# Performance work log

Measured on AMD Instinct MI355X. Metric: run time of the kernel, lower is better.

## Reference

```python
import jax, jax.numpy as jnp
import numpy as np

KERNEL_MUL = 2.0
KERNEL_NUM = 5


def setup_inputs() -> dict:
    key = jax.random.key(0)
    k1, k2 = jax.random.split(key)
    source = jax.random.normal(k1, (4096, 256), dtype=jnp.float32)
    target = jax.random.normal(k2, (4096, 256), dtype=jnp.float32)
    return {"source": source, "target": target}


def reference(source, target):
    n = source.shape[0]
    total = jnp.concatenate([source, target], axis=0)  # [2N, D]
    ns = total.shape[0]
    # Squared-L2 pairwise distances via the GEMM trick (avoids [2N,2N,D] blowup)
    sq = jnp.sum(total * total, axis=1)  # [2N]
    dist = sq[:, None] + sq[None, :] - 2.0 * (total @ total.T)  # [2N,2N]
    # bandwidth computed on detached distances (torch uses .data)
    bandwidth = jax.lax.stop_gradient(jnp.sum(dist)) / (ns * ns - ns)
    bandwidth = bandwidth / (KERNEL_MUL ** (KERNEL_NUM // 2))
    # multi-bandwidth Gaussian kernel sum (small fixed loop over KERNEL_NUM)
    kernels = jnp.zeros_like(dist)
    for i in range(KERNEL_NUM):
        kernels = kernels + jnp.exp(-dist / (bandwidth * (KERNEL_MUL ** i)))
    kernels = kernels / KERNEL_NUM
    XX = kernels[:n, :n]
    YY = kernels[n:, n:]
    XY = kernels[:n, n:]
    YX = kernels[n:, :n]
    # symmetric == 'yes' branch
    return jnp.mean(XX + YY - XY - YX) / 2.0
```

## Files before the change

### kernel.cpp

```cpp
#include <hip/hip_runtime.h>

#define NROWS 8192
#define NHALF 4096
#define DIM   256
#define NB_PREP 256
#define NTILES  64
#define NBLK    2080

typedef __attribute__((ext_vector_type(4))) float f32x4;
typedef __attribute__((ext_vector_type(4))) int   v4i;
typedef __attribute__((ext_vector_type(8))) int   v8i;

__device__ __forceinline__ const float* side_base(const float* src, const float* tgt, int row) {
    return (row < NHALF) ? (src + (size_t)row * DIM)
                         : (tgt + (size_t)(row - NHALF) * DIM);
}

__global__ __launch_bounds__(256) void prep_kernel(
        const float* __restrict__ src, const float* __restrict__ tgt,
        unsigned char* __restrict__ F8,
        float* __restrict__ sq, float* __restrict__ colpart, float* __restrict__ sqpart)
{
    int t = threadIdx.x;
    int lane = t & 63;
    int w = t >> 6;
    int wave = blockIdx.x * 4 + w;
    float cs0 = 0, cs1 = 0, cs2 = 0, cs3 = 0;
    double lss = 0.0;
    for (int r = wave; r < NROWS; r += NB_PREP * 4) {
        const float* p = side_base(src, tgt, r);
        float4 v = *(const float4*)(p + 4 * lane);
        cs0 += v.x; cs1 += v.y; cs2 += v.z; cs3 += v.w;
        int p01 = __builtin_amdgcn_cvt_pk_fp8_f32(v.x, v.y, 0, false);
        int pk  = __builtin_amdgcn_cvt_pk_fp8_f32(v.z, v.w, p01, true);
        *(unsigned*)(F8 + (size_t)r * DIM + 4 * lane) = (unsigned)pk;
        float d = v.x * v.x + v.y * v.y + v.z * v.z + v.w * v.w;
        #pragma unroll
        for (int off = 32; off > 0; off >>= 1) d += __shfl_xor(d, off);
        if (lane == 0) { sq[r] = d; lss += (double)d; }
    }
    __shared__ float csh[4][256];
    __shared__ double ssh[4];
    csh[w][4 * lane + 0] = cs0; csh[w][4 * lane + 1] = cs1;
    csh[w][4 * lane + 2] = cs2; csh[w][4 * lane + 3] = cs3;
    if (lane == 0) ssh[w] = lss;
    __syncthreads();
    colpart[blockIdx.x * 256 + t] = csh[0][t] + csh[1][t] + csh[2][t] + csh[3][t];
    if (t == 0) sqpart[blockIdx.x] = (float)(ssh[0] + ssh[1] + ssh[2] + ssh[3]);
}

__global__ void bw_kernel(const float* __restrict__ colpart,
                          const float* __restrict__ sqpart, float* __restrict__ qconst)
{
    __shared__ double red[256], red2[256];
    int t = threadIdx.x;
    double s = 0;
    for (int b = 0; b < NB_PREP; ++b) s += (double)colpart[b * 256 + t];
    red[t] = s * s;
    red2[t] = (double)sqpart[t];
    __syncthreads();
    for (int k = 128; k > 0; k >>= 1) {
        if (t < k) { red[t] += red[t + k]; red2[t] += red2[t + k]; }
        __syncthreads();
    }
    if (t == 0) {
        double ns = (double)NROWS;
        double sumdist = 2.0 * ns * red2[0] - 2.0 * red[0];
        double bw = sumdist / (ns * ns - ns) / 4.0;
        qconst[0] = (float)(1.4426950408889634 / (16.0 * bw));
    }
}

__device__ __forceinline__ int tri_cum(int b) {
    return b * NTILES - ((b * (b - 1)) >> 1);
}

__device__ __forceinline__ v8i load_frag(const char* base, int r, int kbase) {
    int sw = (r & 7) << 4;
    v4i lo = *(const v4i*)(base + (r << 7) + (kbase ^ sw));
    v4i hi = *(const v4i*)(base + (r << 7) + ((kbase + 16) ^ sw));
    v8i out;
    out[0] = lo[0]; out[1] = lo[1]; out[2] = lo[2]; out[3] = lo[3];
    out[4] = hi[0]; out[5] = hi[1]; out[6] = hi[2]; out[7] = hi[3];
    return out;
}

__device__ __forceinline__ f32x4 mfma_k128(v8i a, v8i b, f32x4 c) {
#if __has_builtin(__builtin_amdgcn_mfma_scale_f32_16x16x128_f8f6f4)
    return __builtin_amdgcn_mfma_scale_f32_16x16x128_f8f6f4(
        a, b, c, 0, 0, 0, 0x7F7F7F7F, 0, 0x7F7F7F7F);
#else
    const long long* av = (const long long*)&a;
    const long long* bv = (const long long*)&b;
    #pragma unroll
    for (int i = 0; i < 4; ++i)
        c = __builtin_amdgcn_mfma_f32_16x16x32_fp8_fp8(av[i], bv[i], c, 0, 0, 0);
    return c;
#endif
}

__global__ __launch_bounds__(256, 4) void mmd_main_kernel(
        const unsigned char* __restrict__ F8,
        const float* __restrict__ sq, const float* __restrict__ qc,
        float* __restrict__ partials)
{
    __shared__ alignas(16) char lds[32768];

    int wg = blockIdx.x;
    int rank = (wg & 7) * (NBLK / 8) + (wg >> 3);
    int by = (int)((129.0f - sqrtf(16641.0f - 8.0f * (float)rank)) * 0.5f);
    while (tri_cum(by + 1) <= rank) ++by;
    while (tri_cum(by) > rank) --by;
    int bx = by + (rank - tri_cum(by));

    int t = threadIdx.x;
    int rowBase = by * 128, colBase = bx * 128;
    int lane = t & 63, w = t >> 6;
    int wr = w >> 1, wc = w & 1;
    int kbase = (lane >> 4) << 5;

    f32x4 acc[4][4];
    #pragma unroll
    for (int m = 0; m < 4; ++m)
        #pragma unroll
        for (int n = 0; n < 4; ++n) acc[m][n] = (f32x4)0.f;

    #pragma unroll
    for (int kc = 0; kc < 2; ++kc) {
        if (kc) __syncthreads();
        #pragma unroll
        for (int q = 0; q < 4; ++q) {
            int p = q * 4096 + t * 16;
            int row = p >> 7;
            int col = (p & 127) ^ ((row & 7) << 4);
            const char* ga = (const char*)F8 + (((size_t)(rowBase + row)) << 8) + kc * 128 + col;
            const char* gb = (const char*)F8 + (((size_t)(colBase + row)) << 8) + kc * 128 + col;
            __builtin_amdgcn_global_load_lds(
                (const __attribute__((address_space(1))) void*)ga,
                (__attribute__((address_space(3))) void*)(lds + p), 16, 0, 0);
            __builtin_amdgcn_global_load_lds(
                (const __attribute__((address_space(1))) void*)gb,
                (__attribute__((address_space(3))) void*)(lds + 16384 + p), 16, 0, 0);
        }
        __syncthreads();

        v8i bf[4];
        #pragma unroll
        for (int n = 0; n < 4; ++n)
            bf[n] = load_frag(lds + 16384, wc * 64 + n * 16 + (lane & 15), kbase);
        #pragma unroll
        for (int m = 0; m < 4; ++m) {
            v8i af = load_frag(lds, wr * 64 + m * 16 + (lane & 15), kbase);
            #pragma unroll
            for (int n = 0; n < 4; ++n)
                acc[m][n] = mfma_k128(af, bf[n], acc[m][n]);
        }
    }

    float q = qc[0], twoq = 2.f * q;
    int rsub = (lane >> 4) * 4, csub = lane & 15;
    float nqa[4][4], qb[4];
    #pragma unroll
    for (int m = 0; m < 4; ++m)
        #pragma unroll
        for (int r = 0; r < 4; ++r)
            nqa[m][r] = -q * sq[rowBase + wr * 64 + m * 16 + rsub + r];
    #pragma unroll
    for (int n = 0; n < 4; ++n)
        qb[n] = q * sq[colBase + wc * 64 + n * 16 + csub];

    float psum = 0.f;
    #pragma unroll
    for (int m = 0; m < 4; ++m) {
        #pragma unroll
        for (int n = 0; n < 4; ++n) {
            #pragma unroll
            for (int r = 0; r < 4; ++r) {
                float arg = fmaf(acc[m][n][r], twoq, nqa[m][r] - qb[n]);
                float e4 = __builtin_amdgcn_exp2f(arg);
                float e3 = e4 * e4, e2 = e3 * e3, e1 = e2 * e2, e0 = e1 * e1;
                psum += ((e4 + e3) + (e2 + e1)) + e0;
            }
        }
    }

    #pragma unroll
    for (int off = 32; off > 0; off >>= 1) psum += __shfl_xor(psum, off);
    __syncthreads();
    float* redw = (float*)lds;
    if (lane == 0) redw[w] = psum;
    __syncthreads();
    if (t == 0) {
        float sign = ((rowBase < NHALF) == (colBase < NHALF)) ? 1.f : -1.f;
        float wgt = (bx == by) ? 1.f : 2.f;
        partials[rank] = sign * wgt * (redw[0] + redw[1] + redw[2] + redw[3]);
    }
}

__global__ void finalize_kernel(const float* __restrict__ partials, int n,
                                float* __restrict__ out)
{
    __shared__ double red[256];
    int t = threadIdx.x;
    double s = 0;
    for (int i = t; i < n; i += 256) s += (double)partials[i];
    red[t] = s;
    __syncthreads();
    for (int k = 128; k > 0; k >>= 1) { if (t < k) red[t] += red[t + k]; __syncthreads(); }
    if (t == 0) {
        double nn = (double)NHALF;
        out[0] = (float)(red[0] / 5.0 / (2.0 * nn * nn));
    }
}

extern "C" void kernel_launch(void* const* d_in, const int* in_sizes, int n_in,
                              void* d_out, int out_size, void* d_ws, size_t ws_size,
                              hipStream_t stream) {
    const float* src = (const float*)d_in[0];
    const float* tgt = (const float*)d_in[1];
    float* out = (float*)d_out;
    char* ws = (char*)d_ws;

    float*         colpart  = (float*)(ws + 0);
    float*         sqpart   = (float*)(ws + 262144);
    float*         qconst   = (float*)(ws + 263168);
    float*         sq       = (float*)(ws + 264192);
    float*         partials = (float*)(ws + 297984);
    unsigned char* F8       = (unsigned char*)(ws + 524288);

    prep_kernel<<<NB_PREP, 256, 0, stream>>>(src, tgt, F8, sq, colpart, sqpart);
    bw_kernel<<<1, 256, 0, stream>>>(colpart, sqpart, qconst);
    mmd_main_kernel<<<NBLK, 256, 0, stream>>>(F8, sq, qconst, partials);
    finalize_kernel<<<1, 256, 0, stream>>>(partials, NBLK, out);
}
```

Baseline: 46.86 us.

## Fuse bandwidth reduction into main kernel, drop LDS staging, pack epilogue math

Removes the single-block bandwidth kernel. The prep kernel now accumulates column sums and the squared-norm total with double atomics into a memset buffer, and every main-kernel block recomputes the exp2 scale from those. The main GEMM loads FP8 fragments straight from global memory into registers instead of staging them through swizzled LDS, and occupancy drops to 3 blocks. The exp epilogue is rewritten with float2 vectors so the compiler can emit packed math. The aim is to cut one launch and LDS traffic, at the cost of redundant global loads, atomics and an extra memset.

```diff
diff --git a/kernel.cpp b/kernel.cpp
--- a/kernel.cpp
+++ b/kernel.cpp
@@ -7,6 +7,7 @@
 #define NTILES  64
 #define NBLK    2080
 
+typedef __attribute__((ext_vector_type(2))) float f32x2;
 typedef __attribute__((ext_vector_type(4))) float f32x4;
 typedef __attribute__((ext_vector_type(4))) int   v4i;
 typedef __attribute__((ext_vector_type(8))) int   v8i;
@@ -18,8 +19,8 @@
 
 __global__ __launch_bounds__(256) void prep_kernel(
         const float* __restrict__ src, const float* __restrict__ tgt,
-        unsigned char* __restrict__ F8,
-        float* __restrict__ sq, float* __restrict__ colpart, float* __restrict__ sqpart)
+        unsigned char* __restrict__ F8, float* __restrict__ sq,
+        double* __restrict__ colsum, double* __restrict__ sumsq)
 {
     int t = threadIdx.x;
     int lane = t & 63;
@@ -45,40 +46,18 @@
     csh[w][4 * lane + 2] = cs2; csh[w][4 * lane + 3] = cs3;
     if (lane == 0) ssh[w] = lss;
     __syncthreads();
-    colpart[blockIdx.x * 256 + t] = csh[0][t] + csh[1][t] + csh[2][t] + csh[3][t];
-    if (t == 0) sqpart[blockIdx.x] = (float)(ssh[0] + ssh[1] + ssh[2] + ssh[3]);
-}
-
-__global__ void bw_kernel(const float* __restrict__ colpart,
-                          const float* __restrict__ sqpart, float* __restrict__ qconst)
-{
-    __shared__ double red[256], red2[256];
-    int t = threadIdx.x;
-    double s = 0;
-    for (int b = 0; b < NB_PREP; ++b) s += (double)colpart[b * 256 + t];
-    red[t] = s * s;
-    red2[t] = (double)sqpart[t];
-    __syncthreads();
-    for (int k = 128; k > 0; k >>= 1) {
-        if (t < k) { red[t] += red[t + k]; red2[t] += red2[t + k]; }
-        __syncthreads();
-    }
-    if (t == 0) {
-        double ns = (double)NROWS;
-        double sumdist = 2.0 * ns * red2[0] - 2.0 * red[0];
-        double bw = sumdist / (ns * ns - ns) / 4.0;
-        qconst[0] = (float)(1.4426950408889634 / (16.0 * bw));
-    }
+    atomicAdd(&colsum[t], (double)(csh[0][t] + csh[1][t] + csh[2][t] + csh[3][t]));
+    if (t == 0) atomicAdd(sumsq, ssh[0] + ssh[1] + ssh[2] + ssh[3]);
 }
 
 __device__ __forceinline__ int tri_cum(int b) {
     return b * NTILES - ((b * (b - 1)) >> 1);
 }
 
-__device__ __forceinline__ v8i load_frag(const char* base, int r, int kbase) {
-    int sw = (r & 7) << 4;
-    v4i lo = *(const v4i*)(base + (r << 7) + (kbase ^ sw));
-    v4i hi = *(const v4i*)(base + (r << 7) + ((kbase + 16) ^ sw));
+__device__ __forceinline__ v8i load_frag_g(const unsigned char* F8, int row, int kcol) {
+    const char* p = (const char*)F8 + ((size_t)row << 8) + kcol;
+    v4i lo = *(const v4i*)p;
+    v4i hi = *(const v4i*)(p + 16);
     v8i out;
     out[0] = lo[0]; out[1] = lo[1]; out[2] = lo[2]; out[3] = lo[3];
     out[4] = hi[0]; out[5] = hi[1]; out[6] = hi[2]; out[7] = hi[3];
@@ -99,12 +78,14 @@
 #endif
 }
 
-__global__ __launch_bounds__(256, 4) void mmd_main_kernel(
-        const unsigned char* __restrict__ F8,
-        const float* __restrict__ sq, const float* __restrict__ qc,
+__global__ __launch_bounds__(256, 3) void mmd_main_kernel(
+        const unsigned char* __restrict__ F8, const float* __restrict__ sq,
+        const double* __restrict__ colsum, const double* __restrict__ sumsq,
         float* __restrict__ partials)
 {
-    __shared__ alignas(16) char lds[32768];
+    __shared__ double qred[4];
+    __shared__ float fred[4];
+    __shared__ float qsh;
 
     int wg = blockIdx.x;
     int rank = (wg & 7) * (NBLK / 8) + (wg >> 3);
@@ -119,6 +100,25 @@
     int wr = w >> 1, wc = w & 1;
     int kbase = (lane >> 4) << 5;
 
+    {
+        double c = colsum[t];
+        double d = c * c;
+        #pragma unroll
+        for (int off = 32; off > 0; off >>= 1) d += __shfl_xor(d, off);
+        if (lane == 0) qred[w] = d;
+        __syncthreads();
+        if (t == 0) {
+            double csq = qred[0] + qred[1] + qred[2] + qred[3];
+            double ns = (double)NROWS;
+            double sumdist = 2.0 * ns * sumsq[0] - 2.0 * csq;
+            double bw = sumdist / (ns * ns - ns) / 4.0;
+            qsh = (float)(1.4426950408889634 / (16.0 * bw));
+        }
+    }
+
+    int arow = rowBase + wr * 64 + (lane & 15);
+    int brow = colBase + wc * 64 + (lane & 15);
+
     f32x4 acc[4][4];
     #pragma unroll
     for (int m = 0; m < 4; ++m)
@@ -127,73 +127,63 @@
 
     #pragma unroll
     for (int kc = 0; kc < 2; ++kc) {
-        if (kc) __syncthreads();
-        #pragma unroll
-        for (int q = 0; q < 4; ++q) {
-            int p = q * 4096 + t * 16;
-            int row = p >> 7;
-            int col = (p & 127) ^ ((row & 7) << 4);
-            const char* ga = (const char*)F8 + (((size_t)(rowBase + row)) << 8) + kc * 128 + col;
-            const char* gb = (const char*)F8 + (((size_t)(colBase + row)) << 8) + kc * 128 + col;
-            __builtin_amdgcn_global_load_lds(
-                (const __attribute__((address_space(1))) void*)ga,
-                (__attribute__((address_space(3))) void*)(lds + p), 16, 0, 0);
-            __builtin_amdgcn_global_load_lds(
-                (const __attribute__((address_space(1))) void*)gb,
-                (__attribute__((address_space(3))) void*)(lds + 16384 + p), 16, 0, 0);
-        }
-        __syncthreads();
-
+        int kcol = kc * 128 + kbase;
         v8i bf[4];
         #pragma unroll
-        for (int n = 0; n < 4; ++n)
-            bf[n] = load_frag(lds + 16384, wc * 64 + n * 16 + (lane & 15), kbase);
+        for (int n = 0; n < 4; ++n) bf[n] = load_frag_g(F8, brow + n * 16, kcol);
         #pragma unroll
         for (int m = 0; m < 4; ++m) {
-            v8i af = load_frag(lds, wr * 64 + m * 16 + (lane & 15), kbase);
+            v8i af = load_frag_g(F8, arow + m * 16, kcol);
             #pragma unroll
             for (int n = 0; n < 4; ++n)
                 acc[m][n] = mfma_k128(af, bf[n], acc[m][n]);
         }
     }
 
-    float q = qc[0], twoq = 2.f * q;
+    __syncthreads();
+    float q = qsh;
+    f32x2 twoq2 = {2.f * q, 2.f * q};
+
     int rsub = (lane >> 4) * 4, csub = lane & 15;
-    float nqa[4][4], qb[4];
+    f32x2 nqa2[4][2];
+    float qb[4];
     #pragma unroll
     for (int m = 0; m < 4; ++m)
         #pragma unroll
-        for (int r = 0; r < 4; ++r)
-            nqa[m][r] = -q * sq[rowBase + wr * 64 + m * 16 + rsub + r];
+        for (int p = 0; p < 2; ++p) {
+            int rr = rowBase + wr * 64 + m * 16 + rsub + 2 * p;
+            nqa2[m][p] = (f32x2){-q * sq[rr], -q * sq[rr + 1]};
+        }
     #pragma unroll
     for (int n = 0; n < 4; ++n)
         qb[n] = q * sq[colBase + wc * 64 + n * 16 + csub];
 
-    float psum = 0.f;
+    f32x2 psum2 = {0.f, 0.f};
     #pragma unroll
     for (int m = 0; m < 4; ++m) {
         #pragma unroll
         for (int n = 0; n < 4; ++n) {
+            f32x2 qbn = {qb[n], qb[n]};
             #pragma unroll
-            for (int r = 0; r < 4; ++r) {
-                float arg = fmaf(acc[m][n][r], twoq, nqa[m][r] - qb[n]);
-                float e4 = __builtin_amdgcn_exp2f(arg);
-                float e3 = e4 * e4, e2 = e3 * e3, e1 = e2 * e2, e0 = e1 * e1;
-                psum += ((e4 + e3) + (e2 + e1)) + e0;
+            for (int p = 0; p < 2; ++p) {
+                f32x2 acc2 = {acc[m][n][2 * p], acc[m][n][2 * p + 1]};
+                f32x2 arg = acc2 * twoq2 + (nqa2[m][p] - qbn);
+                f32x2 e4 = {__builtin_amdgcn_exp2f(arg.x), __builtin_amdgcn_exp2f(arg.y)};
+                f32x2 e3 = e4 * e4, e2 = e3 * e3, e1 = e2 * e2, e0 = e1 * e1;
+                psum2 += ((e4 + e3) + (e2 + e1)) + e0;
             }
         }
     }
+    float psum = psum2.x + psum2.y;
 
     #pragma unroll
     for (int off = 32; off > 0; off >>= 1) psum += __shfl_xor(psum, off);
-    __syncthreads();
-    float* redw = (float*)lds;
-    if (lane == 0) redw[w] = psum;
+    if (lane == 0) fred[w] = psum;
     __syncthreads();
     if (t == 0) {
         float sign = ((rowBase < NHALF) == (colBase < NHALF)) ? 1.f : -1.f;
         float wgt = (bx == by) ? 1.f : 2.f;
-        partials[rank] = sign * wgt * (redw[0] + redw[1] + redw[2] + redw[3]);
+        partials[rank] = sign * wgt * (fred[0] + fred[1] + fred[2] + fred[3]);
     }
 }
 
@@ -221,15 +211,15 @@
     float* out = (float*)d_out;
     char* ws = (char*)d_ws;
 
-    float*         colpart  = (float*)(ws + 0);
-    float*         sqpart   = (float*)(ws + 262144);
-    float*         qconst   = (float*)(ws + 263168);
-    float*         sq       = (float*)(ws + 264192);
-    float*         partials = (float*)(ws + 297984);
+    double*        colsum   = (double*)(ws + 0);
+    double*        sumsq    = (double*)(ws + 2048);
+    float*         sq       = (float*)(ws + 4096);
+    float*         partials = (float*)(ws + 40960);
     unsigned char* F8       = (unsigned char*)(ws + 524288);
 
-    prep_kernel<<<NB_PREP, 256, 0, stream>>>(src, tgt, F8, sq, colpart, sqpart);
-    bw_kernel<<<1, 256, 0, stream>>>(colpart, sqpart, qconst);
-    mmd_main_kernel<<<NBLK, 256, 0, stream>>>(F8, sq, qconst, partials);
+    hipMemsetAsync(ws, 0, 2056, stream);
+
+    prep_kernel<<<NB_PREP, 256, 0, stream>>>(src, tgt, F8, sq, colsum, sumsq);
+    mmd_main_kernel<<<NBLK, 256, 0, stream>>>(F8, sq, colsum, sumsq, partials);
     finalize_kernel<<<1, 256, 0, stream>>>(partials, NBLK, out);
 }
```

Result: slower. 68.25 us (+45.7%).
